# Kernel tuning notes

Measured on AMD Instinct MI355X. Metric: run time of the kernel, lower is better.

## Reference

```python
import jax, jax.numpy as jnp
import numpy as np

N = 100000      # patches per bag
L, H, D = 1024, 512, 256   # size_dict['small']
K = 64          # k_sample
NC = 2          # n_classes


def setup_inputs() -> dict:
    key = jax.random.key(0)
    ks = jax.random.split(key, 12)
    s = 0.02
    return {
        "h": jax.random.normal(ks[0], (N, L), dtype=jnp.float32),
        "W1": jax.random.normal(ks[1], (L, H), dtype=jnp.float32) * s,
        "b1": jnp.zeros((H,), jnp.float32),
        "Wa": jax.random.normal(ks[2], (H, D), dtype=jnp.float32) * s,
        "ba": jnp.zeros((D,), jnp.float32),
        "Wb": jax.random.normal(ks[3], (H, D), dtype=jnp.float32) * s,
        "bb": jnp.zeros((D,), jnp.float32),
        "Wc": jax.random.normal(ks[4], (D, 1), dtype=jnp.float32) * s,
        "bc": jnp.zeros((1,), jnp.float32),
        "Winst": jax.random.normal(ks[5], (H, 2), dtype=jnp.float32) * s,
        "binst": jnp.zeros((2,), jnp.float32),
        "Wcls": jax.random.normal(ks[6], (H, NC), dtype=jnp.float32) * s,
        "bcls": jnp.zeros((NC,), jnp.float32),
        "label": 1,
    }


def reference(h, W1, b1, Wa, ba, Wb, bb, Wc, bc, Winst, binst, Wcls, bcls, label):
    # fc: Linear(1024,512) + ReLU
    h1 = jax.nn.relu(h @ W1 + b1)                      # [N, 512]
    # gated attention net
    a = jnp.tanh(h1 @ Wa + ba)                         # [N, 256]
    g = jax.nn.sigmoid(h1 @ Wb + bb)                   # [N, 256]
    A = (a * g) @ Wc + bc                              # [N, 1]
    A = A.T                                            # [1, N]
    A_raw = A
    A = jax.nn.softmax(A, axis=1)                      # [1, N]

    # instance evaluation: top-k / bottom-k select + gather + tiny classifier
    Asq = A[0]                                         # [N]
    _, top_p_ids = jax.lax.top_k(Asq, K)
    _, top_n_ids = jax.lax.top_k(-Asq, K)
    all_inst = jnp.concatenate([h1[top_p_ids], h1[top_n_ids]], axis=0)  # [2K, 512]
    inst_logits = all_inst @ Winst + binst             # [2K, 2]
    all_preds = jnp.argmax(inst_logits, axis=1)
    p_targets = jnp.full((K,), label, dtype=jnp.int32)
    n_targets = jnp.zeros((K,), dtype=jnp.int32)
    all_targets = jnp.concatenate([p_targets, n_targets], axis=0)
    logp = jax.nn.log_softmax(inst_logits, axis=1)
    instance_loss = -jnp.mean(logp[jnp.arange(2 * K), all_targets])

    # bag-level aggregation and classifier
    M = A @ h1                                         # [1, 512]
    logits = M @ Wcls + bcls                           # [1, n_classes]
    Y_hat = jnp.argmax(logits, axis=1, keepdims=True)
    Y_prob = jax.nn.softmax(logits, axis=1)
    return logits, Y_prob, Y_hat, A_raw, instance_loss, all_preds, all_targets
```

## Files before the change

kernel.cpp:

```cpp
#include <hip/hip_runtime.h>

#define NN 100000
#define LL 1024
#define HH 512
#define DD 256
#define TOPK 64
#define CAP 3072
#define CPB 4
#define DELTA 3e-3f

#define WS_W1T   0u
#define WS_B2    1048576u
#define WS_Z     1572864u
#define Z_MNUM   0u
#define Z_SEXP   2048u
#define Z_LOSS   2052u
#define Z_CNTT   2056u
#define Z_CNTB   2060u
#define Z_HIST   2064u
#define Z_WSA    10256u
#define Z_PARAMS 410384u
#define Z_SEL    410416u
#define Z_CANDT  410928u
#define Z_CANDB  423216u
#define Z_AEXT   435504u
#define Z_AEXB   447792u
#define Z_ZWORDS 108876

typedef float  f32x16 __attribute__((ext_vector_type(16)));
typedef short  bf16x8 __attribute__((ext_vector_type(8)));

#define MFMA(a,b,c) __builtin_amdgcn_mfma_f32_32x32x16_bf16(a,b,c,0,0,0)

__device__ __forceinline__ unsigned short f2bf(float x){
  unsigned u = __float_as_uint(x);
  u += 0x7FFFu + ((u >> 16) & 1u);
  return (unsigned short)(u >> 16);
}
__device__ __forceinline__ float bf2f(unsigned short v){
  return __uint_as_float(((unsigned)v) << 16);
}
__device__ __forceinline__ unsigned sortable_u(float f){
  unsigned u = __float_as_uint(f);
  return (u & 0x80000000u) ? ~u : (u | 0x80000000u);
}
__device__ __forceinline__ float inv_sortable(unsigned u){
  unsigned orig = (u & 0x80000000u) ? (u ^ 0x80000000u) : ~u;
  return __uint_as_float(orig);
}
__device__ __forceinline__ unsigned cvtpk(float lo, float hi){
  unsigned r;
  asm("v_cvt_pk_bf16_f32 %0, %1, %2" : "=v"(r) : "v"(lo), "v"(hi));
  return r;
}

__global__ __launch_bounds__(256)
void k0_prep(const float* __restrict__ W1, const float* __restrict__ Wa,
             const float* __restrict__ Wb,
             unsigned short* __restrict__ W1F, unsigned short* __restrict__ B2F,
             unsigned* __restrict__ zwords)
{
  __shared__ unsigned short T[16 * 512];
  int b = blockIdx.x, tid = threadIdx.x;
  if (b < 64){
    int s = b;
    #pragma unroll
    for (int i = 0; i < 8; ++i){
      int g = tid + 256 * i;
      int kk = g >> 7, c4 = g & 127;
      float4 v = *(const float4*)(W1 + (size_t)(16 * s + kk) * HH + c4 * 4);
      uint2 pk; pk.x = cvtpk(v.x, v.y); pk.y = cvtpk(v.z, v.w);
      *(uint2*)(T + kk * 512 + c4 * 4) = pk;
    }
    __syncthreads();
    int c = tid >> 4, lbase = (tid & 15) * 4;
    #pragma unroll
    for (int q = 0; q < 4; ++q){
      int l = lbase + q; int l31 = l & 31; int kh = l >> 5;
      unsigned short tmp[8];
      #pragma unroll
      for (int j = 0; j < 8; ++j) tmp[j] = T[(kh * 8 + j) * 512 + c * 32 + l31];
      *(bf16x8*)(W1F + ((size_t)(c * 64 + s) * 64 + l) * 8) = *(bf16x8*)tmp;
    }
  } else if (b < 96){
    int s = b - 64;
    #pragma unroll
    for (int i = 0; i < 4; ++i){
      int g = tid + 256 * i;
      int kk = g >> 6, c4 = g & 63;
      float4 va = *(const float4*)(Wa + (size_t)(16 * s + kk) * DD + c4 * 4);
      float4 vb = *(const float4*)(Wb + (size_t)(16 * s + kk) * DD + c4 * 4);
      uint2 pa; pa.x = cvtpk(va.x, va.y); pa.y = cvtpk(va.z, va.w);
      uint2 pb; pb.x = cvtpk(vb.x, vb.y); pb.y = cvtpk(vb.z, vb.w);
      *(uint2*)(T + kk * 512 + c4 * 4) = pa;
      *(uint2*)(T + kk * 512 + 256 + c4 * 4) = pb;
    }
    __syncthreads();
    int c = tid >> 4, lbase = (tid & 15) * 4;
    int col0 = (c & 1) * 256 + (c >> 1) * 32;
    #pragma unroll
    for (int q = 0; q < 4; ++q){
      int l = lbase + q; int l31 = l & 31; int kh = l >> 5;
      unsigned short tmp[8];
      #pragma unroll
      for (int j = 0; j < 8; ++j) tmp[j] = T[(kh * 8 + j) * 512 + col0 + l31];
      *(bf16x8*)(B2F + ((size_t)(c * 32 + s) * 64 + l) * 8) = *(bf16x8*)tmp;
    }
  } else {
    for (int i = (b - 96) * 256 + tid; i < Z_ZWORDS; i += 32 * 256) zwords[i] = 0u;
  }
}

__global__ __launch_bounds__(512, 2)
void k_mega(const float* __restrict__ h, const unsigned short* __restrict__ W1F,
            const unsigned short* __restrict__ B2F,
            const float* __restrict__ b1, const float* __restrict__ ba,
            const float* __restrict__ bbg, const float* __restrict__ Wc,
            const float* __restrict__ bc,
            float* __restrict__ outA,
            float* __restrict__ wsA,
            float* __restrict__ Mnum, float* __restrict__ sum_exp)
{
  __shared__ __align__(16) unsigned short SM[64 * 512];

  const int tid  = threadIdx.x;
  const int wid  = tid >> 6;
  const int lane = tid & 63;
  const int l31  = lane & 31;
  const int half = lane >> 5;
  const int r0   = blockIdx.x * 64;

  const int scol = tid & 63;
  const int srow = tid >> 6;

  const unsigned short* bp = W1F + (size_t)(2 * wid) * 32768 + (size_t)lane * 8;

  f32x16 acc00 = (f32x16)0.f, acc01 = (f32x16)0.f, acc10 = (f32x16)0.f, acc11 = (f32x16)0.f;

  unsigned short* buf0 = SM;
  unsigned short* buf1 = SM + 64 * 256;

  #pragma unroll
  for (int j = 0; j < 8; ++j){
    int r = srow + 8 * j;
    int gr = r0 + r; if (gr > NN - 1) gr = NN - 1;
    float4 v = *(const float4*)(h + (size_t)gr * LL + scol * 4);
    uint2 pk; pk.x = cvtpk(v.x, v.y); pk.y = cvtpk(v.z, v.w);
    *(uint2*)(buf0 + r * 256 + ((((scol >> 1) ^ (r & 31)) << 3) + (scol & 1) * 4)) = pk;
  }
  __syncthreads();

  unsigned short* rb = buf0;
  unsigned short* wb = buf1;

#define SUBIT(i) { \
    const int s0_ = sb + 2 * (i), s1_ = s0_ + 1; \
    bf16x8 b00 = *(const bf16x8*)(bp + s0_ * 512); \
    bf16x8 b01 = *(const bf16x8*)(bp + s1_ * 512); \
    bf16x8 b10 = *(const bf16x8*)(bp + 32768 + s0_ * 512); \
    bf16x8 b11 = *(const bf16x8*)(bp + 32768 + s1_ * 512); \
    const int ck0 = 4 * (i) + half, ck1 = ck0 + 2; \
    bf16x8 a0k0 = *(const bf16x8*)(rb + l31 * 256 + ((ck0 ^ l31) << 3)); \
    bf16x8 a1k0 = *(const bf16x8*)(rb + (32 + l31) * 256 + ((ck0 ^ l31) << 3)); \
    bf16x8 a0k1 = *(const bf16x8*)(rb + l31 * 256 + ((ck1 ^ l31) << 3)); \
    bf16x8 a1k1 = *(const bf16x8*)(rb + (32 + l31) * 256 + ((ck1 ^ l31) << 3)); \
    acc00 = MFMA(a0k0, b00, acc00); acc01 = MFMA(a0k0, b10, acc01); \
    acc10 = MFMA(a1k0, b00, acc10); acc11 = MFMA(a1k0, b10, acc11); \
    acc00 = MFMA(a0k1, b01, acc00); acc01 = MFMA(a0k1, b11, acc01); \
    acc10 = MFMA(a1k1, b01, acc10); acc11 = MFMA(a1k1, b11, acc11); }

#define LDH(dst, j) { \
    int r_ = srow + 8 * (j); \
    int gr_ = r0 + r_; if (gr_ > NN - 1) gr_ = NN - 1; \
    dst = *(const float4*)(h + (size_t)gr_ * LL + coff + scol * 4); }

#define WRH(v, j) { \
    int r_ = srow + 8 * (j); \
    uint2 pk_; pk_.x = cvtpk((v).x, (v).y); pk_.y = cvtpk((v).z, (v).w); \
    *(uint2*)(wb + r_ * 256 + ((((scol >> 1) ^ (r_ & 31)) << 3) + (scol & 1) * 4)) = pk_; }

  #pragma unroll 1
  for (int ch = 0; ch < 4; ++ch){
    const int sb = ch * 16;
    const int coff = (ch + 1) * 256;
    const bool st = (ch < 3);
    float4 hA, hB;
    if (st){ LDH(hA, 0) LDH(hB, 1) }
    SUBIT(0) SUBIT(1)
    if (st){ WRH(hA, 0) WRH(hB, 1) LDH(hA, 2) LDH(hB, 3) }
    SUBIT(2) SUBIT(3)
    if (st){ WRH(hA, 2) WRH(hB, 3) LDH(hA, 4) LDH(hB, 5) }
    SUBIT(4) SUBIT(5)
    if (st){ WRH(hA, 4) WRH(hB, 5) LDH(hA, 6) LDH(hB, 7) }
    SUBIT(6) SUBIT(7)
    if (st){ WRH(hA, 6) WRH(hB, 7) }
    __syncthreads();
    { unsigned short* t = rb; rb = wb; wb = t; }
  }

  {
    float b1v0 = b1[wid * 64 + l31];
    float b1v1 = b1[wid * 64 + 32 + l31];
    int cb0 = wid * 8 + (l31 >> 3);
    int cb1 = wid * 8 + 4 + (l31 >> 3);
    int wi = l31 & 7;
    #pragma unroll
    for (int reg = 0; reg < 16; ++reg){
      int rA = (reg & 3) + ((reg >> 2) << 3) + (half << 2);
      int rB = rA + 32;
      float v;
      v = fmaxf(acc00[reg] + b1v0, 0.f); SM[rA * 512 + ((cb0 ^ (rA & 7)) << 3) + wi] = f2bf(v);
      v = fmaxf(acc01[reg] + b1v1, 0.f); SM[rA * 512 + ((cb1 ^ (rA & 7)) << 3) + wi] = f2bf(v);
      v = fmaxf(acc10[reg] + b1v0, 0.f); SM[rB * 512 + ((cb0 ^ (rB & 7)) << 3) + wi] = f2bf(v);
      v = fmaxf(acc11[reg] + b1v1, 0.f); SM[rB * 512 + ((cb1 ^ (rB & 7)) << 3) + wi] = f2bf(v);
    }
  }
  __syncthreads();

  f32x16 q00 = (f32x16)0.f, q01 = (f32x16)0.f, q10 = (f32x16)0.f, q11 = (f32x16)0.f;
  const unsigned short* p2 = B2F + (size_t)(2 * wid) * 16384 + (size_t)lane * 8;
  const int m0x = l31 & 7;
  #pragma unroll 1
  for (int kc = 0; kc < 16; ++kc){
    #pragma unroll
    for (int ks = 0; ks < 2; ++ks){
      int s = kc * 2 + ks;
      bf16x8 b0 = *(const bf16x8*)(p2 + s * 512);
      bf16x8 b1 = *(const bf16x8*)(p2 + 16384 + s * 512);
      int sw = (((kc * 4 + ks * 2 + half) ^ m0x) << 3);
      bf16x8 a0 = *(const bf16x8*)(SM + l31 * 512 + sw);
      bf16x8 a1 = *(const bf16x8*)(SM + (32 + l31) * 512 + sw);
      q00 = MFMA(a0, b0, q00); q01 = MFMA(a0, b1, q01);
      q10 = MFMA(a1, b0, q10); q11 = MFMA(a1, b1, q11);
    }
  }

  {
    int ca = wid * 32 + l31;
    float bav = ba[ca], bbv = bbg[ca], wcv = Wc[ca];
    #pragma unroll
    for (int mt = 0; mt < 2; ++mt){
      #pragma unroll
      for (int reg = 0; reg < 16; ++reg){
        float pav = (mt ? q10[reg] : q00[reg]) + bav;
        float pbv = (mt ? q11[reg] : q01[reg]) + bbv;
        float p = tanhf(pav) * (1.f / (1.f + expf(-pbv))) * wcv;
        p += __shfl_xor(p, 1, 64);  p += __shfl_xor(p, 2, 64);
        p += __shfl_xor(p, 4, 64);  p += __shfl_xor(p, 8, 64);
        p += __shfl_xor(p, 16, 64);
        if (l31 == 0){
          int rl = mt * 32 + (reg & 3) + ((reg >> 2) << 3) + (half << 2);
          atomicAdd(&wsA[r0 + rl], p);
        }
      }
    }
  }
  __syncthreads();
  if (tid < 64){
    int g = r0 + tid;
    if (g < NN){
      float Ar = atomicAdd(&wsA[g], 0.0f) + bc[0];
      outA[g] = Ar;
    }
  }
  __syncthreads();

  float ev = 0.f;
  { int g = r0 + lane; if (g < NN) ev = expf(outA[g]); }
  float pm = 0.f;
  const int tch = tid >> 3, twi = tid & 7;
  #pragma unroll 4
  for (int r = 0; r < 64; ++r){
    float e = __shfl(ev, r, 64);
    pm += e * bf2f(SM[r * 512 + ((tch ^ (r & 7)) << 3) + twi]);
  }
  atomicAdd(&Mnum[tid], pm);
  if (wid == 0){
    float s = ev;
    s += __shfl_xor(s, 1, 64);  s += __shfl_xor(s, 2, 64);  s += __shfl_xor(s, 4, 64);
    s += __shfl_xor(s, 8, 64);  s += __shfl_xor(s, 16, 64); s += __shfl_xor(s, 32, 64);
    if (lane == 0) atomicAdd(sum_exp, s);
  }
}

__global__ void k_hist(const float* __restrict__ A, unsigned* __restrict__ hist)
{
  __shared__ unsigned lh[2048];
  for (int i = threadIdx.x; i < 2048; i += 256) lh[i] = 0u;
  __syncthreads();
  for (int i = blockIdx.x * 256 + threadIdx.x; i < NN; i += gridDim.x * 256)
    atomicAdd(&lh[sortable_u(A[i]) >> 21], 1u);
  __syncthreads();
  for (int i = threadIdx.x; i < 2048; i += 256)
    if (lh[i]) atomicAdd(&hist[i], lh[i]);
}

__global__ void k_scan(const unsigned* __restrict__ hist, unsigned* __restrict__ params)
{
  if (threadIdx.x == 0){
    unsigned c = 0, hh = 0; int b = 2047;
    for (; b >= 0; --b){ hh = hist[b]; c += hh; if (c >= TOPK) break; }
    if (b < 0) b = 0;
    params[2] = (unsigned)b;
    params[4] = TOPK - (c - hh);
    c = 0; hh = 0; int b2 = 0;
    for (; b2 < 2048; ++b2){ hh = hist[b2]; c += hh; if (c >= TOPK) break; }
    if (b2 > 2047) b2 = 2047;
    params[3] = (unsigned)b2;
    params[5] = TOPK - (c - hh);
  }
}

__global__ void k_hist2(const float* __restrict__ A, const unsigned* __restrict__ params,
                        unsigned* __restrict__ h2T, unsigned* __restrict__ h2B)
{
  __shared__ unsigned lh[4096];
  for (int i = threadIdx.x; i < 4096; i += 256) lh[i] = 0u;
  __syncthreads();
  unsigned bT = params[2], bB = params[3];
  for (int i = blockIdx.x * 256 + threadIdx.x; i < NN; i += gridDim.x * 256){
    unsigned u = sortable_u(A[i]);
    unsigned b = u >> 21;
    if (b == bT) atomicAdd(&lh[(u >> 10) & 2047u], 1u);
    if (b == bB) atomicAdd(&lh[2048 + ((u >> 10) & 2047u)], 1u);
  }
  __syncthreads();
  for (int i = threadIdx.x; i < 2048; i += 256){
    if (lh[i])        atomicAdd(&h2T[i], lh[i]);
    if (lh[2048 + i]) atomicAdd(&h2B[i], lh[2048 + i]);
  }
}

__global__ __launch_bounds__(128)
void k_scan2(const unsigned* __restrict__ h2T, const unsigned* __restrict__ h2B,
             unsigned* __restrict__ params)
{
  int side = threadIdx.x >> 6;
  int lane = threadIdx.x & 63;
  const unsigned* h2 = side ? h2B : h2T;
  unsigned bT  = params[2 + side];
  unsigned rem = params[4 + side];
  unsigned cs = 0;
  int base = lane * 32;
  #pragma unroll 4
  for (int j = 0; j < 32; ++j) cs += h2[base + j];
  unsigned before = 0;
  for (int j = 0; j < 64; ++j){
    unsigned v = __shfl(cs, j, 64);
    bool earlier = side ? (j < lane) : (j > lane);
    if (earlier) before += v;
  }
  if (before < rem && before + cs >= rem){
    unsigned c = before; int s = base;
    if (side == 0){
      for (int b = base + 31; b >= base; --b){ c += h2[b]; if (c >= rem){ s = b; break; } }
      unsigned ulo = (bT << 21) | ((unsigned)s << 10);
      float v = inv_sortable(ulo) - DELTA;
      params[0] = sortable_u(v);
    } else {
      for (int b = base; b < base + 32; ++b){ c += h2[b]; if (c >= rem){ s = b; break; } }
      unsigned uhi = (bT << 21) | ((unsigned)s << 10) | 1023u;
      float v = inv_sortable(uhi) + DELTA;
      params[1] = sortable_u(v);
    }
  }
}

__global__ void k_collect(const float* __restrict__ A, const unsigned* __restrict__ params,
                          unsigned* cntT, unsigned* cntB,
                          unsigned* __restrict__ candT, unsigned* __restrict__ candB)
{
  unsigned p0 = params[0], p1 = params[1];
  for (int i = blockIdx.x * 256 + threadIdx.x; i < NN; i += gridDim.x * 256){
    unsigned u = sortable_u(A[i]);
    if (u >= p0){ unsigned pos = atomicAdd(cntT, 1u); if (pos < CAP) candT[pos] = (unsigned)i; }
    if (u <= p1){ unsigned pos = atomicAdd(cntB, 1u); if (pos < CAP) candB[pos] = (unsigned)i; }
  }
}

__global__ __launch_bounds__(256)
void k_exact(const float* __restrict__ h, const float* __restrict__ W1, const float* __restrict__ b1,
             const float* __restrict__ Wa, const float* __restrict__ ba,
             const float* __restrict__ Wb, const float* __restrict__ bbg,
             const float* __restrict__ Wc, const float* __restrict__ bc,
             const unsigned* cntT, const unsigned* cntB,
             const unsigned* __restrict__ candT, const unsigned* __restrict__ candB,
             float* __restrict__ AexT, float* __restrict__ AexB)
{
  const int PB = CAP / CPB;
  int b = blockIdx.x;
  int side = (b >= PB) ? 1 : 0;
  int base = (side ? b - PB : b) * CPB;
  unsigned cnt = side ? *cntB : *cntT;
  if (cnt > CAP) cnt = CAP;
  if (base >= (int)cnt) return;
  int nc = min(CPB, (int)cnt - base);
  const unsigned* cand = side ? candB : candT;
  float* Aex = side ? AexB : AexT;

  __shared__ float hrow[CPB][LL];
  __shared__ float h1row[CPB][HH];
  __shared__ unsigned rows_s[CPB];
  __shared__ float red[4][CPB];
  int tid = threadIdx.x;
  if (tid < CPB) rows_s[tid] = cand[base + min(tid, nc - 1)];
  __syncthreads();
  for (int c = 0; c < CPB; ++c)
    ((float4*)hrow[c])[tid] = ((const float4*)(h + (size_t)rows_s[c] * LL))[tid];
  __syncthreads();

  float s0[CPB], s1[CPB];
  { float v0 = b1[tid], v1 = b1[tid + 256];
    #pragma unroll
    for (int c = 0; c < CPB; ++c){ s0[c] = v0; s1[c] = v1; } }
  for (int k = 0; k < LL; ++k){
    float w0 = W1[k * HH + tid];
    float w1 = W1[k * HH + tid + 256];
    #pragma unroll
    for (int c = 0; c < CPB; ++c){ float hv = hrow[c][k]; s0[c] += hv * w0; s1[c] += hv * w1; }
  }
  #pragma unroll
  for (int c = 0; c < CPB; ++c){
    h1row[c][tid] = fmaxf(s0[c], 0.f);
    h1row[c][tid + 256] = fmaxf(s1[c], 0.f);
  }
  __syncthreads();

  float pa[CPB], pb[CPB];
  float bav = ba[tid], bbv = bbg[tid], wcv = Wc[tid];
  #pragma unroll
  for (int c = 0; c < CPB; ++c){ pa[c] = bav; pb[c] = bbv; }
  for (int k = 0; k < HH; ++k){
    float wav = Wa[k * DD + tid];
    float wbv = Wb[k * DD + tid];
    #pragma unroll
    for (int c = 0; c < CPB; ++c){ float hv = h1row[c][k]; pa[c] += hv * wav; pb[c] += hv * wbv; }
  }
  int lane = tid & 63, w = tid >> 6;
  #pragma unroll
  for (int c = 0; c < CPB; ++c){
    float p = tanhf(pa[c]) * (1.f / (1.f + expf(-pb[c]))) * wcv;
    p += __shfl_xor(p, 1, 64);  p += __shfl_xor(p, 2, 64);  p += __shfl_xor(p, 4, 64);
    p += __shfl_xor(p, 8, 64);  p += __shfl_xor(p, 16, 64); p += __shfl_xor(p, 32, 64);
    if (lane == 0) red[w][c] = p;
  }
  __syncthreads();
  if (tid == 0)
    for (int c = 0; c < nc; ++c)
      Aex[base + c] = red[0][c] + red[1][c] + red[2][c] + red[3][c] + bc[0];
}

__global__ __launch_bounds__(256)
void k_select(const unsigned* cntT, const unsigned* cntB,
              const unsigned* __restrict__ candT, const unsigned* __restrict__ candB,
              const float* __restrict__ AexT, const float* __restrict__ AexB,
              unsigned* __restrict__ sel)
{
  __shared__ unsigned long long keys[CAP];
  __shared__ unsigned long long wmax[4];
  __shared__ unsigned long long best_s;
  int tid = threadIdx.x;
  for (int side = 0; side < 2; ++side){
    unsigned cnt = side ? *cntB : *cntT; if (cnt > CAP) cnt = CAP;
    const unsigned* cand = side ? candB : candT;
    const float* Aex = side ? AexB : AexT;
    for (int j = tid; j < (int)cnt; j += 256){
      unsigned su = sortable_u(Aex[j]);
      if (side) su = ~su;
      keys[j] = (((unsigned long long)su) << 32) | (unsigned long long)(0xFFFFFFFFu - cand[j]);
    }
    __syncthreads();
    for (int it = 0; it < TOPK; ++it){
      unsigned long long loc = 0ull;
      for (int j = tid; j < (int)cnt; j += 256){ unsigned long long k = keys[j]; loc = (k > loc) ? k : loc; }
      for (int off = 1; off < 64; off <<= 1){
        unsigned long long o = __shfl_xor(loc, off, 64);
        loc = (o > loc) ? o : loc;
      }
      if ((tid & 63) == 0) wmax[tid >> 6] = loc;
      __syncthreads();
      if (tid == 0){
        unsigned long long m01 = (wmax[0] > wmax[1]) ? wmax[0] : wmax[1];
        unsigned long long m23 = (wmax[2] > wmax[3]) ? wmax[2] : wmax[3];
        unsigned long long bb_ = (m01 > m23) ? m01 : m23;
        best_s = bb_;
        sel[side * TOPK + it] = 0xFFFFFFFFu - (unsigned)(bb_ & 0xFFFFFFFFull);
      }
      __syncthreads();
      unsigned long long bv = best_s;
      for (int j = tid; j < (int)cnt; j += 256) if (keys[j] == bv) keys[j] = 0ull;
      __syncthreads();
    }
    __syncthreads();
  }
}

__global__ __launch_bounds__(256)
void k_inst(const float* __restrict__ h, const float* __restrict__ W1, const float* __restrict__ b1,
            const float* __restrict__ Winst, const float* __restrict__ binst,
            const unsigned* __restrict__ sel, const int* __restrict__ labelp,
            float* __restrict__ out, float* __restrict__ loss_sum)
{
  __shared__ float hrow[LL];
  __shared__ float h1row[HH];
  __shared__ float red[4][2];
  int i = blockIdx.x, tid = threadIdx.x;
  unsigned row = sel[i];
  ((float4*)hrow)[tid] = ((const float4*)(h + (size_t)row * LL))[tid];
  __syncthreads();
  float s0 = b1[tid], s1 = b1[tid + 256];
  for (int k = 0; k < LL; ++k){
    float hv = hrow[k];
    s0 += hv * W1[k * HH + tid];
    s1 += hv * W1[k * HH + tid + 256];
  }
  h1row[tid] = fmaxf(s0, 0.f); h1row[tid + 256] = fmaxf(s1, 0.f);
  __syncthreads();
  float l0 = 0.f, l1 = 0.f;
  for (int d = tid; d < HH; d += 256){
    float hv = h1row[d];
    l0 += hv * Winst[d * 2];
    l1 += hv * Winst[d * 2 + 1];
  }
  for (int off = 1; off < 64; off <<= 1){ l0 += __shfl_xor(l0, off, 64); l1 += __shfl_xor(l1, off, 64); }
  if ((tid & 63) == 0){ red[tid >> 6][0] = l0; red[tid >> 6][1] = l1; }
  __syncthreads();
  if (tid == 0){
    float L0 = red[0][0] + red[1][0] + red[2][0] + red[3][0] + binst[0];
    float L1 = red[0][1] + red[1][1] + red[2][1] + red[3][1] + binst[1];
    int lab = labelp[0];
    int tgt = (i < TOPK) ? lab : 0;
    out[100006 + i] = (L1 > L0) ? 1.f : 0.f;
    out[100134 + i] = (float)tgt;
    float m = fmaxf(L0, L1);
    float lse = m + logf(expf(L0 - m) + expf(L1 - m));
    float lp = ((tgt == 1) ? L1 : L0) - lse;
    atomicAdd(loss_sum, -lp);
  }
}

__global__ __launch_bounds__(512)
void k_final(const float* __restrict__ Mnum, const float* __restrict__ sum_exp,
             const float* __restrict__ Wcls, const float* __restrict__ bcls,
             const float* __restrict__ loss_sum, float* __restrict__ out)
{
  __shared__ float red[8][2];
  int tid = threadIdx.x;
  float S = *sum_exp;
  float m = Mnum[tid] / S;
  float p0 = m * Wcls[tid * 2], p1 = m * Wcls[tid * 2 + 1];
  for (int off = 1; off < 64; off <<= 1){ p0 += __shfl_xor(p0, off, 64); p1 += __shfl_xor(p1, off, 64); }
  if ((tid & 63) == 0){ red[tid >> 6][0] = p0; red[tid >> 6][1] = p1; }
  __syncthreads();
  if (tid == 0){
    float L0 = bcls[0], L1 = bcls[1];
    for (int w = 0; w < 8; ++w){ L0 += red[w][0]; L1 += red[w][1]; }
    out[0] = L0; out[1] = L1;
    float mm = fmaxf(L0, L1);
    float e0 = expf(L0 - mm), e1 = expf(L1 - mm);
    out[2] = e0 / (e0 + e1); out[3] = e1 / (e0 + e1);
    out[4] = (L1 > L0) ? 1.f : 0.f;
    out[100005] = loss_sum[0] / 128.f;
  }
}

extern "C" void kernel_launch(void* const* d_in, const int* in_sizes, int n_in,
                              void* d_out, int out_size, void* d_ws, size_t ws_size,
                              hipStream_t stream)
{
  const float* h     = (const float*)d_in[0];
  const float* W1    = (const float*)d_in[1];
  const float* b1    = (const float*)d_in[2];
  const float* Wa    = (const float*)d_in[3];
  const float* ba    = (const float*)d_in[4];
  const float* Wb    = (const float*)d_in[5];
  const float* bbg   = (const float*)d_in[6];
  const float* Wc    = (const float*)d_in[7];
  const float* bc    = (const float*)d_in[8];
  const float* Winst = (const float*)d_in[9];
  const float* binst = (const float*)d_in[10];
  const float* Wcls  = (const float*)d_in[11];
  const float* bcls  = (const float*)d_in[12];
  const int*   label = (const int*)d_in[13];
  float* out = (float*)d_out;

  char* ws = (char*)d_ws;
  unsigned short* W1F = (unsigned short*)(ws + WS_W1T);
  unsigned short* B2F = (unsigned short*)(ws + WS_B2);
  char* Z = ws + WS_Z;
  float*    Mnum   = (float*)(Z + Z_MNUM);
  float*    sexp   = (float*)(Z + Z_SEXP);
  float*    lsum   = (float*)(Z + Z_LOSS);
  unsigned* cntT   = (unsigned*)(Z + Z_CNTT);
  unsigned* cntB   = (unsigned*)(Z + Z_CNTB);
  unsigned* hist   = (unsigned*)(Z + Z_HIST);
  float*    wsA    = (float*)(Z + Z_WSA);
  unsigned* params = (unsigned*)(Z + Z_PARAMS);
  unsigned* sel    = (unsigned*)(Z + Z_SEL);
  unsigned* candT  = (unsigned*)(Z + Z_CANDT);
  unsigned* candB  = (unsigned*)(Z + Z_CANDB);
  float*    AexT   = (float*)(Z + Z_AEXT);
  float*    AexB   = (float*)(Z + Z_AEXB);
  unsigned* h2T    = (unsigned*)(Z + Z_CANDT);
  unsigned* h2B    = (unsigned*)(Z + Z_CANDB);

  k0_prep<<<128, 256, 0, stream>>>(W1, Wa, Wb, W1F, B2F, (unsigned*)Z);
  k_mega<<<1563, 512, 0, stream>>>(h, W1F, B2F, b1, ba, bbg, Wc, bc,
                                   out + 5, wsA, Mnum, sexp);
  k_hist<<<400, 256, 0, stream>>>(out + 5, hist);
  k_scan<<<1, 64, 0, stream>>>(hist, params);
  k_hist2<<<400, 256, 0, stream>>>(out + 5, params, h2T, h2B);
  k_scan2<<<1, 128, 0, stream>>>(h2T, h2B, params);
  k_collect<<<400, 256, 0, stream>>>(out + 5, params, cntT, cntB, candT, candB);
  k_exact<<<2 * (CAP / CPB), 256, 0, stream>>>(h, W1, b1, Wa, ba, Wb, bbg, Wc, bc,
                                               cntT, cntB, candT, candB, AexT, AexB);
  k_select<<<1, 256, 0, stream>>>(cntT, cntB, candT, candB, AexT, AexB, sel);
  k_inst<<<128, 256, 0, stream>>>(h, W1, b1, Winst, binst, sel, label, out, lsum);
  k_final<<<1, 512, 0, stream>>>(Mnum, sexp, Wcls, bcls, lsum, out);
}
```

Baseline: 1.101 ms.

## Fuse post-attention selection pipeline into one cooperative kernel with grid syncs

```diff
diff --git a/kernel.cpp b/kernel.cpp
--- a/kernel.cpp
+++ b/kernel.cpp
@@ -1,4 +1,7 @@
 #include <hip/hip_runtime.h>
+#include <hip/hip_cooperative_groups.h>
+
+namespace cg = cooperative_groups;
 
 #define NN 100000
 #define LL 1024
@@ -6,7 +9,6 @@
 #define DD 256
 #define TOPK 64
 #define CAP 3072
-#define CPB 4
 #define DELTA 3e-3f
 
 #define WS_W1T   0u
@@ -119,7 +121,8 @@
             const float* __restrict__ bc,
             float* __restrict__ outA,
             float* __restrict__ wsA,
-            float* __restrict__ Mnum, float* __restrict__ sum_exp)
+            float* __restrict__ Mnum, float* __restrict__ sum_exp,
+            unsigned* __restrict__ histg)
 {
   __shared__ __align__(16) unsigned short SM[64 * 512];
 
@@ -261,6 +264,7 @@
     if (g < NN){
       float Ar = atomicAdd(&wsA[g], 0.0f) + bc[0];
       outA[g] = Ar;
+      atomicAdd(&histg[sortable_u(Ar) >> 21], 1u);
     }
   }
   __syncthreads();
@@ -283,284 +287,253 @@
   }
 }
 
-__global__ void k_hist(const float* __restrict__ A, unsigned* __restrict__ hist)
+struct CoopArgs {
+  const float* h; const float* W1; const float* b1;
+  const float* Wa; const float* ba; const float* Wb; const float* bbg;
+  const float* Wc; const float* bc;
+  const float* Winst; const float* binst; const float* Wcls; const float* bcls;
+  const int* label;
+  float* out; float* A;
+  unsigned* hist; unsigned* params; unsigned* h2T; unsigned* h2B;
+  unsigned* cntT; unsigned* cntB; unsigned* candT; unsigned* candB;
+  float* AexT; float* AexB; unsigned* sel;
+  float* Mnum; float* sexp; float* lsum;
+};
+
+#define CGRID 256
+
+__global__ __launch_bounds__(256, 1)
+void k_coop(CoopArgs a)
 {
-  __shared__ unsigned lh[2048];
-  for (int i = threadIdx.x; i < 2048; i += 256) lh[i] = 0u;
-  __syncthreads();
-  for (int i = blockIdx.x * 256 + threadIdx.x; i < NN; i += gridDim.x * 256)
-    atomicAdd(&lh[sortable_u(A[i]) >> 21], 1u);
-  __syncthreads();
-  for (int i = threadIdx.x; i < 2048; i += 256)
-    if (lh[i]) atomicAdd(&hist[i], lh[i]);
-}
-
-__global__ void k_scan(const unsigned* __restrict__ hist, unsigned* __restrict__ params)
-{
-  if (threadIdx.x == 0){
-    unsigned c = 0, hh = 0; int b = 2047;
-    for (; b >= 0; --b){ hh = hist[b]; c += hh; if (c >= TOPK) break; }
-    if (b < 0) b = 0;
-    params[2] = (unsigned)b;
-    params[4] = TOPK - (c - hh);
-    c = 0; hh = 0; int b2 = 0;
-    for (; b2 < 2048; ++b2){ hh = hist[b2]; c += hh; if (c >= TOPK) break; }
-    if (b2 > 2047) b2 = 2047;
-    params[3] = (unsigned)b2;
-    params[5] = TOPK - (c - hh);
-  }
-}
-
-__global__ void k_hist2(const float* __restrict__ A, const unsigned* __restrict__ params,
-                        unsigned* __restrict__ h2T, unsigned* __restrict__ h2B)
-{
-  __shared__ unsigned lh[4096];
-  for (int i = threadIdx.x; i < 4096; i += 256) lh[i] = 0u;
-  __syncthreads();
-  unsigned bT = params[2], bB = params[3];
-  for (int i = blockIdx.x * 256 + threadIdx.x; i < NN; i += gridDim.x * 256){
-    unsigned u = sortable_u(A[i]);
-    unsigned b = u >> 21;
-    if (b == bT) atomicAdd(&lh[(u >> 10) & 2047u], 1u);
-    if (b == bB) atomicAdd(&lh[2048 + ((u >> 10) & 2047u)], 1u);
-  }
-  __syncthreads();
-  for (int i = threadIdx.x; i < 2048; i += 256){
-    if (lh[i])        atomicAdd(&h2T[i], lh[i]);
-    if (lh[2048 + i]) atomicAdd(&h2B[i], lh[2048 + i]);
-  }
-}
-
-__global__ __launch_bounds__(128)
-void k_scan2(const unsigned* __restrict__ h2T, const unsigned* __restrict__ h2B,
-             unsigned* __restrict__ params)
-{
-  int side = threadIdx.x >> 6;
-  int lane = threadIdx.x & 63;
-  const unsigned* h2 = side ? h2B : h2T;
-  unsigned bT  = params[2 + side];
-  unsigned rem = params[4 + side];
-  unsigned cs = 0;
-  int base = lane * 32;
-  #pragma unroll 4
-  for (int j = 0; j < 32; ++j) cs += h2[base + j];
-  unsigned before = 0;
-  for (int j = 0; j < 64; ++j){
-    unsigned v = __shfl(cs, j, 64);
-    bool earlier = side ? (j < lane) : (j > lane);
-    if (earlier) before += v;
-  }
-  if (before < rem && before + cs >= rem){
-    unsigned c = before; int s = base;
-    if (side == 0){
-      for (int b = base + 31; b >= base; --b){ c += h2[b]; if (c >= rem){ s = b; break; } }
-      unsigned ulo = (bT << 21) | ((unsigned)s << 10);
-      float v = inv_sortable(ulo) - DELTA;
-      params[0] = sortable_u(v);
-    } else {
-      for (int b = base; b < base + 32; ++b){ c += h2[b]; if (c >= rem){ s = b; break; } }
-      unsigned uhi = (bT << 21) | ((unsigned)s << 10) | 1023u;
-      float v = inv_sortable(uhi) + DELTA;
-      params[1] = sortable_u(v);
-    }
-  }
-}
-
-__global__ void k_collect(const float* __restrict__ A, const unsigned* __restrict__ params,
-                          unsigned* cntT, unsigned* cntB,
-                          unsigned* __restrict__ candT, unsigned* __restrict__ candB)
-{
-  unsigned p0 = params[0], p1 = params[1];
-  for (int i = blockIdx.x * 256 + threadIdx.x; i < NN; i += gridDim.x * 256){
-    unsigned u = sortable_u(A[i]);
-    if (u >= p0){ unsigned pos = atomicAdd(cntT, 1u); if (pos < CAP) candT[pos] = (unsigned)i; }
-    if (u <= p1){ unsigned pos = atomicAdd(cntB, 1u); if (pos < CAP) candB[pos] = (unsigned)i; }
-  }
-}
-
-__global__ __launch_bounds__(256)
-void k_exact(const float* __restrict__ h, const float* __restrict__ W1, const float* __restrict__ b1,
-             const float* __restrict__ Wa, const float* __restrict__ ba,
-             const float* __restrict__ Wb, const float* __restrict__ bbg,
-             const float* __restrict__ Wc, const float* __restrict__ bc,
-             const unsigned* cntT, const unsigned* cntB,
-             const unsigned* __restrict__ candT, const unsigned* __restrict__ candB,
-             float* __restrict__ AexT, float* __restrict__ AexB)
-{
-  const int PB = CAP / CPB;
-  int b = blockIdx.x;
-  int side = (b >= PB) ? 1 : 0;
-  int base = (side ? b - PB : b) * CPB;
-  unsigned cnt = side ? *cntB : *cntT;
-  if (cnt > CAP) cnt = CAP;
-  if (base >= (int)cnt) return;
-  int nc = min(CPB, (int)cnt - base);
-  const unsigned* cand = side ? candB : candT;
-  float* Aex = side ? AexB : AexT;
-
-  __shared__ float hrow[CPB][LL];
-  __shared__ float h1row[CPB][HH];
-  __shared__ unsigned rows_s[CPB];
-  __shared__ float red[4][CPB];
-  int tid = threadIdx.x;
-  if (tid < CPB) rows_s[tid] = cand[base + min(tid, nc - 1)];
-  __syncthreads();
-  for (int c = 0; c < CPB; ++c)
-    ((float4*)hrow[c])[tid] = ((const float4*)(h + (size_t)rows_s[c] * LL))[tid];
-  __syncthreads();
-
-  float s0[CPB], s1[CPB];
-  { float v0 = b1[tid], v1 = b1[tid + 256];
-    #pragma unroll
-    for (int c = 0; c < CPB; ++c){ s0[c] = v0; s1[c] = v1; } }
-  for (int k = 0; k < LL; ++k){
-    float w0 = W1[k * HH + tid];
-    float w1 = W1[k * HH + tid + 256];
-    #pragma unroll
-    for (int c = 0; c < CPB; ++c){ float hv = hrow[c][k]; s0[c] += hv * w0; s1[c] += hv * w1; }
-  }
-  #pragma unroll
-  for (int c = 0; c < CPB; ++c){
-    h1row[c][tid] = fmaxf(s0[c], 0.f);
-    h1row[c][tid + 256] = fmaxf(s1[c], 0.f);
-  }
-  __syncthreads();
-
-  float pa[CPB], pb[CPB];
-  float bav = ba[tid], bbv = bbg[tid], wcv = Wc[tid];
-  #pragma unroll
-  for (int c = 0; c < CPB; ++c){ pa[c] = bav; pb[c] = bbv; }
-  for (int k = 0; k < HH; ++k){
-    float wav = Wa[k * DD + tid];
-    float wbv = Wb[k * DD + tid];
-    #pragma unroll
-    for (int c = 0; c < CPB; ++c){ float hv = h1row[c][k]; pa[c] += hv * wav; pb[c] += hv * wbv; }
-  }
-  int lane = tid & 63, w = tid >> 6;
-  #pragma unroll
-  for (int c = 0; c < CPB; ++c){
-    float p = tanhf(pa[c]) * (1.f / (1.f + expf(-pb[c]))) * wcv;
-    p += __shfl_xor(p, 1, 64);  p += __shfl_xor(p, 2, 64);  p += __shfl_xor(p, 4, 64);
-    p += __shfl_xor(p, 8, 64);  p += __shfl_xor(p, 16, 64); p += __shfl_xor(p, 32, 64);
-    if (lane == 0) red[w][c] = p;
-  }
-  __syncthreads();
-  if (tid == 0)
-    for (int c = 0; c < nc; ++c)
-      Aex[base + c] = red[0][c] + red[1][c] + red[2][c] + red[3][c] + bc[0];
-}
-
-__global__ __launch_bounds__(256)
-void k_select(const unsigned* cntT, const unsigned* cntB,
-              const unsigned* __restrict__ candT, const unsigned* __restrict__ candB,
-              const float* __restrict__ AexT, const float* __restrict__ AexB,
-              unsigned* __restrict__ sel)
-{
-  __shared__ unsigned long long keys[CAP];
-  __shared__ unsigned long long wmax[4];
-  __shared__ unsigned long long best_s;
-  int tid = threadIdx.x;
-  for (int side = 0; side < 2; ++side){
-    unsigned cnt = side ? *cntB : *cntT; if (cnt > CAP) cnt = CAP;
-    const unsigned* cand = side ? candB : candT;
-    const float* Aex = side ? AexB : AexT;
-    for (int j = tid; j < (int)cnt; j += 256){
-      unsigned su = sortable_u(Aex[j]);
-      if (side) su = ~su;
-      keys[j] = (((unsigned long long)su) << 32) | (unsigned long long)(0xFFFFFFFFu - cand[j]);
-    }
-    __syncthreads();
-    for (int it = 0; it < TOPK; ++it){
-      unsigned long long loc = 0ull;
-      for (int j = tid; j < (int)cnt; j += 256){ unsigned long long k = keys[j]; loc = (k > loc) ? k : loc; }
-      for (int off = 1; off < 64; off <<= 1){
-        unsigned long long o = __shfl_xor(loc, off, 64);
-        loc = (o > loc) ? o : loc;
-      }
-      if ((tid & 63) == 0) wmax[tid >> 6] = loc;
+  cg::grid_group grid = cg::this_grid();
+  const int tid = threadIdx.x;
+  const int bid = blockIdx.x;
+  __shared__ __align__(16) char SMEM[24640];
+
+  if (bid == 0){
+    unsigned* lh = (unsigned*)SMEM;
+    for (int i = tid; i < 2048; i += 256) lh[i] = a.hist[i];
+    __syncthreads();
+    if (tid == 0){
+      unsigned c = 0, hh = 0; int b = 2047;
+      for (; b >= 0; --b){ hh = lh[b]; c += hh; if (c >= TOPK) break; }
+      if (b < 0) b = 0;
+      a.params[2] = (unsigned)b; a.params[4] = TOPK - (c - hh);
+      c = 0; hh = 0; int b2 = 0;
+      for (; b2 < 2048; ++b2){ hh = lh[b2]; c += hh; if (c >= TOPK) break; }
+      if (b2 > 2047) b2 = 2047;
+      a.params[3] = (unsigned)b2; a.params[5] = TOPK - (c - hh);
+    }
+  }
+  grid.sync();
+
+  {
+    unsigned* lh = (unsigned*)SMEM;
+    for (int i = tid; i < 4096; i += 256) lh[i] = 0u;
+    __syncthreads();
+    unsigned bT = a.params[2], bB = a.params[3];
+    for (int i = bid * 256 + tid; i < NN; i += CGRID * 256){
+      unsigned u = sortable_u(a.A[i]);
+      unsigned b = u >> 21;
+      if (b == bT) atomicAdd(&lh[(u >> 10) & 2047u], 1u);
+      if (b == bB) atomicAdd(&lh[2048 + ((u >> 10) & 2047u)], 1u);
+    }
+    __syncthreads();
+    for (int i = tid; i < 2048; i += 256){
+      if (lh[i])        atomicAdd(&a.h2T[i], lh[i]);
+      if (lh[2048 + i]) atomicAdd(&a.h2B[i], lh[2048 + i]);
+    }
+  }
+  grid.sync();
+
+  if (bid == 0){
+    unsigned* lh = (unsigned*)SMEM;
+    for (int i = tid; i < 2048; i += 256){ lh[i] = a.h2T[i]; lh[2048 + i] = a.h2B[i]; }
+    __syncthreads();
+    if (tid < 128){
+      int side = tid >> 6;
+      int lane = tid & 63;
+      const unsigned* h2 = lh + side * 2048;
+      unsigned bT  = a.params[2 + side];
+      unsigned rem = a.params[4 + side];
+      unsigned cs = 0;
+      int base = lane * 32;
+      #pragma unroll 4
+      for (int j = 0; j < 32; ++j) cs += h2[base + j];
+      unsigned before = 0;
+      for (int j = 0; j < 64; ++j){
+        unsigned v = __shfl(cs, j, 64);
+        bool earlier = side ? (j < lane) : (j > lane);
+        if (earlier) before += v;
+      }
+      if (before < rem && before + cs >= rem){
+        unsigned c = before; int s = base;
+        if (side == 0){
+          for (int b = base + 31; b >= base; --b){ c += h2[b]; if (c >= rem){ s = b; break; } }
+          unsigned ulo = (bT << 21) | ((unsigned)s << 10);
+          float v = inv_sortable(ulo) - DELTA;
+          a.params[0] = sortable_u(v);
+        } else {
+          for (int b = base; b < base + 32; ++b){ c += h2[b]; if (c >= rem){ s = b; break; } }
+          unsigned uhi = (bT << 21) | ((unsigned)s << 10) | 1023u;
+          float v = inv_sortable(uhi) + DELTA;
+          a.params[1] = sortable_u(v);
+        }
+      }
+    }
+  }
+  grid.sync();
+
+  {
+    unsigned p0 = a.params[0], p1 = a.params[1];
+    for (int i = bid * 256 + tid; i < NN; i += CGRID * 256){
+      unsigned u = sortable_u(a.A[i]);
+      if (u >= p0){ unsigned pos = atomicAdd(a.cntT, 1u); if (pos < CAP) a.candT[pos] = (unsigned)i; }
+      if (u <= p1){ unsigned pos = atomicAdd(a.cntB, 1u); if (pos < CAP) a.candB[pos] = (unsigned)i; }
+    }
+  }
+  grid.sync();
+
+  {
+    unsigned cT = *a.cntT; if (cT > CAP) cT = CAP;
+    unsigned cB = *a.cntB; if (cB > CAP) cB = CAP;
+    int tot = (int)(cT + cB);
+    float* hrow  = (float*)SMEM;
+    float* h1row = (float*)(SMEM + 4096);
+    float* red   = (float*)(SMEM + 6144);
+    for (int r = bid; r < tot; r += CGRID){
+      int side = (r >= (int)cT);
+      int j = side ? r - (int)cT : r;
+      unsigned row = side ? a.candB[j] : a.candT[j];
       __syncthreads();
-      if (tid == 0){
-        unsigned long long m01 = (wmax[0] > wmax[1]) ? wmax[0] : wmax[1];
-        unsigned long long m23 = (wmax[2] > wmax[3]) ? wmax[2] : wmax[3];
-        unsigned long long bb_ = (m01 > m23) ? m01 : m23;
-        best_s = bb_;
-        sel[side * TOPK + it] = 0xFFFFFFFFu - (unsigned)(bb_ & 0xFFFFFFFFull);
-      }
+      ((float4*)hrow)[tid] = ((const float4*)(a.h + (size_t)row * LL))[tid];
       __syncthreads();
-      unsigned long long bv = best_s;
-      for (int j = tid; j < (int)cnt; j += 256) if (keys[j] == bv) keys[j] = 0ull;
+      float s0 = a.b1[tid], s1 = a.b1[tid + 256];
+      for (int k = 0; k < LL; ++k){
+        float hv = hrow[k];
+        s0 += hv * a.W1[k * HH + tid];
+        s1 += hv * a.W1[k * HH + tid + 256];
+      }
+      h1row[tid] = fmaxf(s0, 0.f); h1row[tid + 256] = fmaxf(s1, 0.f);
       __syncthreads();
-    }
-    __syncthreads();
-  }
-}
-
-__global__ __launch_bounds__(256)
-void k_inst(const float* __restrict__ h, const float* __restrict__ W1, const float* __restrict__ b1,
-            const float* __restrict__ Winst, const float* __restrict__ binst,
-            const unsigned* __restrict__ sel, const int* __restrict__ labelp,
-            float* __restrict__ out, float* __restrict__ loss_sum)
-{
-  __shared__ float hrow[LL];
-  __shared__ float h1row[HH];
-  __shared__ float red[4][2];
-  int i = blockIdx.x, tid = threadIdx.x;
-  unsigned row = sel[i];
-  ((float4*)hrow)[tid] = ((const float4*)(h + (size_t)row * LL))[tid];
-  __syncthreads();
-  float s0 = b1[tid], s1 = b1[tid + 256];
-  for (int k = 0; k < LL; ++k){
-    float hv = hrow[k];
-    s0 += hv * W1[k * HH + tid];
-    s1 += hv * W1[k * HH + tid + 256];
-  }
-  h1row[tid] = fmaxf(s0, 0.f); h1row[tid + 256] = fmaxf(s1, 0.f);
-  __syncthreads();
-  float l0 = 0.f, l1 = 0.f;
-  for (int d = tid; d < HH; d += 256){
-    float hv = h1row[d];
-    l0 += hv * Winst[d * 2];
-    l1 += hv * Winst[d * 2 + 1];
-  }
-  for (int off = 1; off < 64; off <<= 1){ l0 += __shfl_xor(l0, off, 64); l1 += __shfl_xor(l1, off, 64); }
-  if ((tid & 63) == 0){ red[tid >> 6][0] = l0; red[tid >> 6][1] = l1; }
-  __syncthreads();
-  if (tid == 0){
-    float L0 = red[0][0] + red[1][0] + red[2][0] + red[3][0] + binst[0];
-    float L1 = red[0][1] + red[1][1] + red[2][1] + red[3][1] + binst[1];
-    int lab = labelp[0];
-    int tgt = (i < TOPK) ? lab : 0;
-    out[100006 + i] = (L1 > L0) ? 1.f : 0.f;
-    out[100134 + i] = (float)tgt;
-    float m = fmaxf(L0, L1);
-    float lse = m + logf(expf(L0 - m) + expf(L1 - m));
-    float lp = ((tgt == 1) ? L1 : L0) - lse;
-    atomicAdd(loss_sum, -lp);
-  }
-}
-
-__global__ __launch_bounds__(512)
-void k_final(const float* __restrict__ Mnum, const float* __restrict__ sum_exp,
-             const float* __restrict__ Wcls, const float* __restrict__ bcls,
-             const float* __restrict__ loss_sum, float* __restrict__ out)
-{
-  __shared__ float red[8][2];
-  int tid = threadIdx.x;
-  float S = *sum_exp;
-  float m = Mnum[tid] / S;
-  float p0 = m * Wcls[tid * 2], p1 = m * Wcls[tid * 2 + 1];
-  for (int off = 1; off < 64; off <<= 1){ p0 += __shfl_xor(p0, off, 64); p1 += __shfl_xor(p1, off, 64); }
-  if ((tid & 63) == 0){ red[tid >> 6][0] = p0; red[tid >> 6][1] = p1; }
-  __syncthreads();
-  if (tid == 0){
-    float L0 = bcls[0], L1 = bcls[1];
-    for (int w = 0; w < 8; ++w){ L0 += red[w][0]; L1 += red[w][1]; }
-    out[0] = L0; out[1] = L1;
-    float mm = fmaxf(L0, L1);
-    float e0 = expf(L0 - mm), e1 = expf(L1 - mm);
-    out[2] = e0 / (e0 + e1); out[3] = e1 / (e0 + e1);
-    out[4] = (L1 > L0) ? 1.f : 0.f;
-    out[100005] = loss_sum[0] / 128.f;
+      float pa = a.ba[tid], pb = a.bbg[tid];
+      for (int k = 0; k < HH; ++k){
+        float hv = h1row[k];
+        pa += hv * a.Wa[k * DD + tid];
+        pb += hv * a.Wb[k * DD + tid];
+      }
+      float p = tanhf(pa) * (1.f / (1.f + expf(-pb))) * a.Wc[tid];
+      p += __shfl_xor(p, 1, 64);  p += __shfl_xor(p, 2, 64);  p += __shfl_xor(p, 4, 64);
+      p += __shfl_xor(p, 8, 64);  p += __shfl_xor(p, 16, 64); p += __shfl_xor(p, 32, 64);
+      if ((tid & 63) == 0) red[tid >> 6] = p;
+      __syncthreads();
+      if (tid == 0)
+        (side ? a.AexB : a.AexT)[j] = red[0] + red[1] + red[2] + red[3] + a.bc[0];
+    }
+  }
+  grid.sync();
+
+  if (bid == 0){
+    unsigned long long* keys = (unsigned long long*)SMEM;
+    unsigned long long* wmax = (unsigned long long*)(SMEM + 24576);
+    __shared__ unsigned long long best_s;
+    for (int side = 0; side < 2; ++side){
+      unsigned cnt = side ? *a.cntB : *a.cntT; if (cnt > CAP) cnt = CAP;
+      const unsigned* cand = side ? a.candB : a.candT;
+      const float* Aex = side ? a.AexB : a.AexT;
+      for (int j = tid; j < (int)cnt; j += 256){
+        unsigned su = sortable_u(Aex[j]);
+        if (side) su = ~su;
+        keys[j] = (((unsigned long long)su) << 32) | (unsigned long long)(0xFFFFFFFFu - cand[j]);
+      }
+      __syncthreads();
+      for (int it = 0; it < TOPK; ++it){
+        unsigned long long loc = 0ull;
+        for (int j = tid; j < (int)cnt; j += 256){ unsigned long long k = keys[j]; loc = (k > loc) ? k : loc; }
+        for (int off = 1; off < 64; off <<= 1){
+          unsigned long long o = __shfl_xor(loc, off, 64);
+          loc = (o > loc) ? o : loc;
+        }
+        if ((tid & 63) == 0) wmax[tid >> 6] = loc;
+        __syncthreads();
+        if (tid == 0){
+          unsigned long long m01 = (wmax[0] > wmax[1]) ? wmax[0] : wmax[1];
+          unsigned long long m23 = (wmax[2] > wmax[3]) ? wmax[2] : wmax[3];
+          unsigned long long bb_ = (m01 > m23) ? m01 : m23;
+          best_s = bb_;
+          a.sel[side * TOPK + it] = 0xFFFFFFFFu - (unsigned)(bb_ & 0xFFFFFFFFull);
+        }
+        __syncthreads();
+        unsigned long long bv = best_s;
+        for (int j = tid; j < (int)cnt; j += 256) if (keys[j] == bv) keys[j] = 0ull;
+        __syncthreads();
+      }
+      __syncthreads();
+    }
+  }
+  grid.sync();
+
+  if (bid < 128){
+    float* hrow  = (float*)SMEM;
+    float* h1row = (float*)(SMEM + 4096);
+    float* red   = (float*)(SMEM + 6144);
+    unsigned row = a.sel[bid];
+    ((float4*)hrow)[tid] = ((const float4*)(a.h + (size_t)row * LL))[tid];
+    __syncthreads();
+    float s0 = a.b1[tid], s1 = a.b1[tid + 256];
+    for (int k = 0; k < LL; ++k){
+      float hv = hrow[k];
+      s0 += hv * a.W1[k * HH + tid];
+      s1 += hv * a.W1[k * HH + tid + 256];
+    }
+    h1row[tid] = fmaxf(s0, 0.f); h1row[tid + 256] = fmaxf(s1, 0.f);
+    __syncthreads();
+    float l0 = 0.f, l1 = 0.f;
+    for (int d = tid; d < HH; d += 256){
+      float hv = h1row[d];
+      l0 += hv * a.Winst[d * 2];
+      l1 += hv * a.Winst[d * 2 + 1];
+    }
+    for (int off = 1; off < 64; off <<= 1){ l0 += __shfl_xor(l0, off, 64); l1 += __shfl_xor(l1, off, 64); }
+    if ((tid & 63) == 0){ red[(tid >> 6) * 2] = l0; red[(tid >> 6) * 2 + 1] = l1; }
+    __syncthreads();
+    if (tid == 0){
+      float L0 = red[0] + red[2] + red[4] + red[6] + a.binst[0];
+      float L1 = red[1] + red[3] + red[5] + red[7] + a.binst[1];
+      int lab = a.label[0];
+      int tgt = (bid < TOPK) ? lab : 0;
+      a.out[100006 + bid] = (L1 > L0) ? 1.f : 0.f;
+      a.out[100134 + bid] = (float)tgt;
+      float m = fmaxf(L0, L1);
+      float lse = m + logf(expf(L0 - m) + expf(L1 - m));
+      float lp = ((tgt == 1) ? L1 : L0) - lse;
+      atomicAdd(a.lsum, -lp);
+    }
+  }
+  grid.sync();
+
+  if (bid == 0){
+    float* red = (float*)SMEM;
+    float S = *a.sexp;
+    float p0 = 0.f, p1 = 0.f;
+    for (int c = tid; c < HH; c += 256){
+      float m = a.Mnum[c] / S;
+      p0 += m * a.Wcls[c * 2];
+      p1 += m * a.Wcls[c * 2 + 1];
+    }
+    for (int off = 1; off < 64; off <<= 1){ p0 += __shfl_xor(p0, off, 64); p1 += __shfl_xor(p1, off, 64); }
+    if ((tid & 63) == 0){ red[(tid >> 6) * 2] = p0; red[(tid >> 6) * 2 + 1] = p1; }
+    __syncthreads();
+    if (tid == 0){
+      float L0 = a.bcls[0] + red[0] + red[2] + red[4] + red[6];
+      float L1 = a.bcls[1] + red[1] + red[3] + red[5] + red[7];
+      a.out[0] = L0; a.out[1] = L1;
+      float mm = fmaxf(L0, L1);
+      float e0 = expf(L0 - mm), e1 = expf(L1 - mm);
+      a.out[2] = e0 / (e0 + e1); a.out[3] = e1 / (e0 + e1);
+      a.out[4] = (L1 > L0) ? 1.f : 0.f;
+      a.out[100005] = atomicAdd(a.lsum, 0.0f) / 128.f;
+    }
   }
 }
 
@@ -606,15 +579,16 @@
 
   k0_prep<<<128, 256, 0, stream>>>(W1, Wa, Wb, W1F, B2F, (unsigned*)Z);
   k_mega<<<1563, 512, 0, stream>>>(h, W1F, B2F, b1, ba, bbg, Wc, bc,
-                                   out + 5, wsA, Mnum, sexp);
-  k_hist<<<400, 256, 0, stream>>>(out + 5, hist);
-  k_scan<<<1, 64, 0, stream>>>(hist, params);
-  k_hist2<<<400, 256, 0, stream>>>(out + 5, params, h2T, h2B);
-  k_scan2<<<1, 128, 0, stream>>>(h2T, h2B, params);
-  k_collect<<<400, 256, 0, stream>>>(out + 5, params, cntT, cntB, candT, candB);
-  k_exact<<<2 * (CAP / CPB), 256, 0, stream>>>(h, W1, b1, Wa, ba, Wb, bbg, Wc, bc,
-                                               cntT, cntB, candT, candB, AexT, AexB);
-  k_select<<<1, 256, 0, stream>>>(cntT, cntB, candT, candB, AexT, AexB, sel);
-  k_inst<<<128, 256, 0, stream>>>(h, W1, b1, Winst, binst, sel, label, out, lsum);
-  k_final<<<1, 512, 0, stream>>>(Mnum, sexp, Wcls, bcls, lsum, out);
-}
+                                   out + 5, wsA, Mnum, sexp, hist);
+
+  CoopArgs ca;
+  ca.h = h; ca.W1 = W1; ca.b1 = b1; ca.Wa = Wa; ca.ba = ba; ca.Wb = Wb; ca.bbg = bbg;
+  ca.Wc = Wc; ca.bc = bc; ca.Winst = Winst; ca.binst = binst; ca.Wcls = Wcls; ca.bcls = bcls;
+  ca.label = label; ca.out = out; ca.A = out + 5;
+  ca.hist = hist; ca.params = params; ca.h2T = h2T; ca.h2B = h2B;
+  ca.cntT = cntT; ca.cntB = cntB; ca.candT = candT; ca.candB = candB;
+  ca.AexT = AexT; ca.AexB = AexB; ca.sel = sel;
+  ca.Mnum = Mnum; ca.sexp = sexp; ca.lsum = lsum;
+  void* kargs[] = { (void*)&ca };
+  hipLaunchCooperativeKernel(k_coop, dim3(CGRID), dim3(256), kargs, 0, stream);
+}
```

New measurement: 1.291 ms. 17.3% more time.
